# Performance work log

Hardware: AMD Instinct MI355X
Metric: run time of the kernel (lower is better)

Reference implementation:

```python
import jax, jax.numpy as jnp
import numpy as np

B, D, H, O, E = 16384, 256, 256, 256, 32
N_ACTIVE = 22          # int(32 * 0.7) from BoltzmannGate
TEMP = float(np.e)     # Boltzmann temperature
EPS = 1e-8


def setup_inputs() -> dict:
    key = jax.random.key(0)
    ks = jax.random.split(key, 7)
    s = 0.02  # init scale for weights
    return {
        "x":  jax.random.normal(ks[0], (B, D), dtype=jnp.float32),
        "W1": jax.random.normal(ks[1], (E, H, D), dtype=jnp.float32) * s,  # [E, out=H, in=D] torch Linear layout
        "b1": jax.random.normal(ks[2], (E, H), dtype=jnp.float32) * s,
        "W2": jax.random.normal(ks[3], (E, O, H), dtype=jnp.float32) * s,
        "b2": jax.random.normal(ks[4], (E, O), dtype=jnp.float32) * s,
        "Wg": jax.random.normal(ks[5], (E, D), dtype=jnp.float32) * s,
        "bg": jax.random.normal(ks[6], (E,), dtype=jnp.float32) * s,
    }


def reference(x, W1, b1, W2, b2, Wg, bg):
    # Dense all-experts forward: [B, E, H] -> relu -> [B, E, O]
    h = jax.nn.relu(jnp.einsum('bd,ehd->beh', x, W1) + b1[None, :, :])
    expert_out = jnp.einsum('beh,eoh->beo', h, W2) + b2[None, :, :]

    # Boltzmann gate: softmax(scores / T), keep top-k probs, renormalize.
    scores = (x @ Wg.T + bg) / TEMP                      # [B, E]
    probs = jax.nn.softmax(scores, axis=-1)
    _, topk_idx = jax.lax.top_k(probs, N_ACTIVE)         # [B, N_ACTIVE]
    mask = jnp.zeros_like(probs).at[jnp.arange(B)[:, None], topk_idx].set(1.0)
    weights = probs * mask
    weights = weights / (jnp.sum(weights, axis=-1, keepdims=True) + EPS)

    # Weighted combine over experts: [B, O]
    return jnp.einsum('be,beo->bo', weights, expert_out)
```

## Files before the change

kernel.cpp:

```cpp
#include <hip/hip_runtime.h>
#include <hip/hip_bf16.h>


typedef __attribute__((ext_vector_type(8))) short bf16x8;
typedef __attribute__((ext_vector_type(4))) float f32x4;

__device__ __forceinline__ unsigned short f2bf(float f) {
    unsigned u = __builtin_bit_cast(unsigned, f);
    u += 0x7FFFu + ((u >> 16) & 1u);
    return (unsigned short)(u >> 16);
}
__device__ __forceinline__ unsigned pack_bf16x2(float a, float b) {
    return (unsigned)f2bf(a) | ((unsigned)f2bf(b) << 16);
}

#define LX(r, ch) (((r) << 8) + ((((ch) ^ ((r) & 7))) << 3))

__global__ __launch_bounds__(256) void cvt_w(const float* __restrict__ W1,
                                             const float* __restrict__ W2,
                                             unsigned short* __restrict__ Wr) {
    int T = blockIdx.x * 256 + threadIdx.x;
    int lane = T & 63, t = (T >> 6) & 1, kb = (T >> 7) & 7;
    int s = (T >> 10) & 15, e = T >> 14;
    int l15 = lane & 15, quad = lane >> 4;
    int row = (s & 7) * 32 + t * 16 + l15;
    const float* src = ((s < 8) ? W1 : W2) +
                       ((long)e * 256 + row) * 256 + kb * 32 + quad * 8;
    float4 v0 = ((const float4*)src)[0], v1 = ((const float4*)src)[1];
    uint4 o;
    o.x = pack_bf16x2(v0.x, v0.y); o.y = pack_bf16x2(v0.z, v0.w);
    o.z = pack_bf16x2(v1.x, v1.y); o.w = pack_bf16x2(v1.z, v1.w);
    ((uint4*)Wr)[T] = o;
}

__global__ __launch_bounds__(1024, 4) void moe_kernel(
    const float* __restrict__ x,
    const unsigned short* __restrict__ Wr,
    const float* __restrict__ bias1,
    const float* __restrict__ b2,
    const float* __restrict__ Wg,
    const float* __restrict__ bg,
    float* __restrict__ out)
{
    __shared__ __align__(16) unsigned short x_s[64 * 256];
    __shared__ __align__(16) unsigned short h_s[2][64 * 256];
    __shared__ float gws[64 * 33];

    const int tid  = threadIdx.x;
    const int wv   = tid >> 6, lane = tid & 63;
    const int quad = lane >> 4, l15 = lane & 15;
    const int crew = wv >> 3, g = wv & 7;
    const int row0 = blockIdx.x * 64;

#pragma unroll
    for (int c = 0; c < 2; ++c) {
        int chunk = tid + c * 1024;
        int r = chunk >> 5, ch = chunk & 31;
        const float4* s = (const float4*)(x + (long)(row0 + r) * 256 + ch * 8);
        float4 v0 = s[0], v1 = s[1];
        uint4 o;
        o.x = pack_bf16x2(v0.x, v0.y); o.y = pack_bf16x2(v0.z, v0.w);
        o.z = pack_bf16x2(v1.x, v1.y); o.w = pack_bf16x2(v1.z, v1.w);
        *(uint4*)(&x_s[LX(r, ch)]) = o;
    }

    {
        const int e32 = lane & 31, half = lane >> 5;
        const float4* wg4 = (const float4*)(Wg + e32 * 256 + half * 128);
        float bgv = bg[e32];
        for (int i = 0; i < 4; ++i) {
            int lr = wv * 4 + i;
            const float4* xr4 = (const float4*)(x + (long)(row0 + lr) * 256 + half * 128);
            float acc = 0.f;
#pragma unroll
            for (int tt = 0; tt < 32; ++tt) {
                float4 w = wg4[tt], xv = xr4[tt];
                acc = fmaf(w.x, xv.x, acc); acc = fmaf(w.y, xv.y, acc);
                acc = fmaf(w.z, xv.z, acc); acc = fmaf(w.w, xv.w, acc);
            }
            acc += __shfl_xor(acc, 32);
            float score = (acc + bgv) / 2.71828182845904523f;

            float m = score;
#pragma unroll
            for (int d = 16; d >= 1; d >>= 1) m = fmaxf(m, __shfl_xor(m, d));
            float p = expf(score - m);
            float ps = p;
#pragma unroll
            for (int d = 16; d >= 1; d >>= 1) ps += __shfl_xor(ps, d);
            float prob = p / ps;

            int rank = 0;
#pragma unroll
            for (int j = 0; j < 32; ++j) {
                float pj = __shfl(prob, j);
                rank += (pj > prob || (pj == prob && j < e32)) ? 1 : 0;
            }
            float kept = (rank < 22) ? prob : 0.f;
            float wsum = kept;
#pragma unroll
            for (int d = 16; d >= 1; d >>= 1) wsum += __shfl_xor(wsum, d);
            float weight = kept / (wsum + 1e-8f);

            if (half == 0) gws[lr * 33 + e32] = weight;
        }
    }

    __syncthreads();

    f32x4 oacc[2][4];
#pragma unroll
    for (int ot = 0; ot < 2; ++ot)
#pragma unroll
        for (int rt = 0; rt < 4; ++rt) {
            f32x4 z = {0.f, 0.f, 0.f, 0.f};
            oacc[ot][rt] = z;
        }
    if (crew == 1) {
        for (int ee = 0; ee < 32; ++ee) {
            float gv[4];
#pragma unroll
            for (int rt = 0; rt < 4; ++rt) gv[rt] = gws[(rt * 16 + l15) * 33 + ee];
#pragma unroll
            for (int ot = 0; ot < 2; ++ot) {
                float4 bb = *(const float4*)(b2 + ee * 256 + g * 32 + ot * 16 + quad * 4);
#pragma unroll
                for (int rt = 0; rt < 4; ++rt) {
                    oacc[ot][rt][0] = fmaf(gv[rt], bb.x, oacc[ot][rt][0]);
                    oacc[ot][rt][1] = fmaf(gv[rt], bb.y, oacc[ot][rt][1]);
                    oacc[ot][rt][2] = fmaf(gv[rt], bb.z, oacc[ot][rt][2]);
                    oacc[ot][rt][3] = fmaf(gv[rt], bb.w, oacc[ot][rt][3]);
                }
            }
        }
    }

    bf16x8 buf[2][2];
    {
        const unsigned short* p0 = Wr + (long)wv * 8192;
        buf[0][0] = *(const bf16x8*)(p0 + lane * 8);
        buf[0][1] = *(const bf16x8*)(p0 + 512 + lane * 8);
        buf[1][0] = *(const bf16x8*)(p0 + 1024 + lane * 8);
        buf[1][1] = *(const bf16x8*)(p0 + 1536 + lane * 8);
    }

    for (int e = 0; e <= 32; ++e) {
        if (crew == 0) {
            if (e < 32) {
                f32x4 hacc[2][4];
#pragma unroll
                for (int ht = 0; ht < 2; ++ht)
#pragma unroll
                    for (int rt = 0; rt < 4; ++rt) {
                        f32x4 z = {0.f, 0.f, 0.f, 0.f};
                        hacc[ht][rt] = z;
                    }
                const unsigned short* w_e = Wr + ((long)(e * 16 + wv) * 8) * 1024;
#pragma unroll
                for (int kb = 0; kb < 8; ++kb) {
                    bf16x8 a0 = buf[kb & 1][0], a1 = buf[kb & 1][1];
                    const unsigned short* np =
                        w_e + ((kb < 6) ? (kb + 2) : (128 + kb - 6)) * 1024;
                    buf[kb & 1][0] = *(const bf16x8*)(np + lane * 8);
                    buf[kb & 1][1] = *(const bf16x8*)(np + 512 + lane * 8);
                    bf16x8 bbv[4];
#pragma unroll
                    for (int rt = 0; rt < 4; ++rt)
                        bbv[rt] = *(const bf16x8*)(&x_s[LX(rt * 16 + l15, kb * 4 + quad)]);
                    __builtin_amdgcn_s_setprio(1);
#pragma unroll
                    for (int rt = 0; rt < 4; ++rt) {
                        hacc[0][rt] = __builtin_amdgcn_mfma_f32_16x16x32_bf16(
                            a0, bbv[rt], hacc[0][rt], 0, 0, 0);
                        hacc[1][rt] = __builtin_amdgcn_mfma_f32_16x16x32_bf16(
                            a1, bbv[rt], hacc[1][rt], 0, 0, 0);
                    }
                    __builtin_amdgcn_s_setprio(0);
                }
                unsigned short* hb = h_s[e & 1];
                float4 bv[2]; float gw[4];
#pragma unroll
                for (int ht = 0; ht < 2; ++ht)
                    bv[ht] = *(const float4*)(bias1 + e * 256 + g * 32 + ht * 16 + quad * 4);
#pragma unroll
                for (int rt = 0; rt < 4; ++rt)
                    gw[rt] = gws[(rt * 16 + l15) * 33 + e];
#pragma unroll
                for (int ht = 0; ht < 2; ++ht) {
                    int hcol = g * 32 + ht * 16 + quad * 4;
                    int ch = hcol >> 3, off = hcol & 7;
#pragma unroll
                    for (int rt = 0; rt < 4; ++rt) {
                        int r = rt * 16 + l15;
                        float v0 = fmaxf(hacc[ht][rt][0] + bv[ht].x, 0.f) * gw[rt];
                        float v1 = fmaxf(hacc[ht][rt][1] + bv[ht].y, 0.f) * gw[rt];
                        float v2 = fmaxf(hacc[ht][rt][2] + bv[ht].z, 0.f) * gw[rt];
                        float v3 = fmaxf(hacc[ht][rt][3] + bv[ht].w, 0.f) * gw[rt];
                        uint2 pk;
                        pk.x = pack_bf16x2(v0, v1);
                        pk.y = pack_bf16x2(v2, v3);
                        *(uint2*)(&hb[(r << 8) + ((ch ^ (r & 7)) << 3) + off]) = pk;
                    }
                }
            }
        } else {
            if (e >= 1) {
                const int me = e - 1;
                const unsigned short* w_e = Wr + ((long)(me * 16 + wv) * 8) * 1024;
                const unsigned short* hbuf = h_s[me & 1];
#pragma unroll
                for (int kb = 0; kb < 8; ++kb) {
                    bf16x8 a0 = buf[kb & 1][0], a1 = buf[kb & 1][1];
                    const unsigned short* np =
                        w_e + ((kb < 6) ? (kb + 2) : (128 + kb - 6)) * 1024;
                    buf[kb & 1][0] = *(const bf16x8*)(np + lane * 8);
                    buf[kb & 1][1] = *(const bf16x8*)(np + 512 + lane * 8);
                    bf16x8 bbv[4];
#pragma unroll
                    for (int rt = 0; rt < 4; ++rt)
                        bbv[rt] = *(const bf16x8*)(&hbuf[LX(rt * 16 + l15, kb * 4 + quad)]);
                    __builtin_amdgcn_s_setprio(1);
#pragma unroll
                    for (int rt = 0; rt < 4; ++rt) {
                        oacc[0][rt] = __builtin_amdgcn_mfma_f32_16x16x32_bf16(
                            a0, bbv[rt], oacc[0][rt], 0, 0, 0);
                        oacc[1][rt] = __builtin_amdgcn_mfma_f32_16x16x32_bf16(
                            a1, bbv[rt], oacc[1][rt], 0, 0, 0);
                    }
                    __builtin_amdgcn_s_setprio(0);
                }
            }
        }

        __syncthreads();
    }

    if (crew == 1) {
#pragma unroll
        for (int ot = 0; ot < 2; ++ot)
#pragma unroll
            for (int rt = 0; rt < 4; ++rt)
                *(f32x4*)(out + (long)(row0 + rt * 16 + l15) * 256 +
                          g * 32 + ot * 16 + quad * 4) = oacc[ot][rt];
    }
}

extern "C" void kernel_launch(void* const* d_in, const int* in_sizes, int n_in,
                              void* d_out, int out_size, void* d_ws, size_t ws_size,
                              hipStream_t stream) {
    (void)in_sizes; (void)n_in; (void)out_size; (void)ws_size;
    const float* x  = (const float*)d_in[0];
    const float* W1 = (const float*)d_in[1];
    const float* b1 = (const float*)d_in[2];
    const float* W2 = (const float*)d_in[3];
    const float* b2 = (const float*)d_in[4];
    const float* Wg = (const float*)d_in[5];
    const float* bg = (const float*)d_in[6];
    float* out = (float*)d_out;

    unsigned short* Wr = (unsigned short*)d_ws;

    cvt_w<<<2048, 256, 0, stream>>>(W1, W2, Wr);
    moe_kernel<<<256, 1024, 0, stream>>>(x, Wr, b1, b2, Wg, bg, out);
}
```

Measured before the change: 304.8 us.

## Merge GEMM1/GEMM2 crews so every wave interleaves both stages per expert

Before, the 16 waves were split into two crews: one computed the first GEMM (hidden) and the other the second GEMM (output). Now every wave handles a 16-column slice of both, interleaving GEMM1 for expert e with GEMM2 for expert e-1 inside one k-loop. The aim is to balance MFMA load across all waves and hide each stage's latency with the other's instructions. The converted weight layout becomes a per-wave contiguous stream padded to 33 experts, with a 4-deep register prefetch ring. The full __syncthreads is swapped for an explicit lgkmcnt wait plus s_barrier, and the b2 bias prologue is now spread over all waves.

Measured after the change: 546.6 us. 79.3% more time.

```diff
diff --git a/kernel.cpp b/kernel.cpp
--- a/kernel.cpp
+++ b/kernel.cpp
@@ -20,18 +20,48 @@
                                              const float* __restrict__ W2,
                                              unsigned short* __restrict__ Wr) {
     int T = blockIdx.x * 256 + threadIdx.x;
-    int lane = T & 63, t = (T >> 6) & 1, kb = (T >> 7) & 7;
-    int s = (T >> 10) & 15, e = T >> 14;
+    int lane = T & 63, kb = (T >> 6) & 7, e = (T >> 9) & 31;
+    int s = (T >> 14) & 15, m = T >> 18;
     int l15 = lane & 15, quad = lane >> 4;
-    int row = (s & 7) * 32 + t * 16 + l15;
-    const float* src = ((s < 8) ? W1 : W2) +
-                       ((long)e * 256 + row) * 256 + kb * 32 + quad * 8;
+    const float* src = (m ? W2 : W1) +
+                       ((long)e * 256 + s * 16 + l15) * 256 + kb * 32 + quad * 8;
     float4 v0 = ((const float4*)src)[0], v1 = ((const float4*)src)[1];
     uint4 o;
     o.x = pack_bf16x2(v0.x, v0.y); o.y = pack_bf16x2(v0.z, v0.w);
     o.z = pack_bf16x2(v1.x, v1.y); o.w = pack_bf16x2(v1.z, v1.w);
-    ((uint4*)Wr)[T] = o;
-}
+    long U = (((long)(m * 16 + s) * 33 + e) * 8 + kb) * 64 + lane;
+    ((uint4*)Wr)[U] = o;
+}
+
+#define G1STEP(kb) do {                                                        \
+    bf16x8 a = r1[(kb) & 3];                                                   \
+    r1[(kb) & 3] = *(const bf16x8*)(w1p + (e * 8 + (kb) + 4) * 512);           \
+    bf16x8 xb0 = *(const bf16x8*)(&x_s[LX(l15,      (kb) * 4 + quad)]);        \
+    bf16x8 xb1 = *(const bf16x8*)(&x_s[LX(16 + l15, (kb) * 4 + quad)]);        \
+    bf16x8 xb2 = *(const bf16x8*)(&x_s[LX(32 + l15, (kb) * 4 + quad)]);        \
+    bf16x8 xb3 = *(const bf16x8*)(&x_s[LX(48 + l15, (kb) * 4 + quad)]);        \
+    __builtin_amdgcn_s_setprio(1);                                             \
+    hacc[0] = __builtin_amdgcn_mfma_f32_16x16x32_bf16(a, xb0, hacc[0], 0, 0, 0); \
+    hacc[1] = __builtin_amdgcn_mfma_f32_16x16x32_bf16(a, xb1, hacc[1], 0, 0, 0); \
+    hacc[2] = __builtin_amdgcn_mfma_f32_16x16x32_bf16(a, xb2, hacc[2], 0, 0, 0); \
+    hacc[3] = __builtin_amdgcn_mfma_f32_16x16x32_bf16(a, xb3, hacc[3], 0, 0, 0); \
+    __builtin_amdgcn_s_setprio(0);                                             \
+} while (0)
+
+#define G2STEP(kb) do {                                                        \
+    bf16x8 a = r2[(kb) & 3];                                                   \
+    r2[(kb) & 3] = *(const bf16x8*)(w2p + (me * 8 + (kb) + 4) * 512);          \
+    bf16x8 hb0 = *(const bf16x8*)(&hbr[LX(l15,      (kb) * 4 + quad)]);        \
+    bf16x8 hb1 = *(const bf16x8*)(&hbr[LX(16 + l15, (kb) * 4 + quad)]);        \
+    bf16x8 hb2 = *(const bf16x8*)(&hbr[LX(32 + l15, (kb) * 4 + quad)]);        \
+    bf16x8 hb3 = *(const bf16x8*)(&hbr[LX(48 + l15, (kb) * 4 + quad)]);        \
+    __builtin_amdgcn_s_setprio(1);                                             \
+    oacc[0] = __builtin_amdgcn_mfma_f32_16x16x32_bf16(a, hb0, oacc[0], 0, 0, 0); \
+    oacc[1] = __builtin_amdgcn_mfma_f32_16x16x32_bf16(a, hb1, oacc[1], 0, 0, 0); \
+    oacc[2] = __builtin_amdgcn_mfma_f32_16x16x32_bf16(a, hb2, oacc[2], 0, 0, 0); \
+    oacc[3] = __builtin_amdgcn_mfma_f32_16x16x32_bf16(a, hb3, oacc[3], 0, 0, 0); \
+    __builtin_amdgcn_s_setprio(0);                                             \
+} while (0)
 
 __global__ __launch_bounds__(1024, 4) void moe_kernel(
     const float* __restrict__ x,
@@ -49,7 +79,6 @@
     const int tid  = threadIdx.x;
     const int wv   = tid >> 6, lane = tid & 63;
     const int quad = lane >> 4, l15 = lane & 15;
-    const int crew = wv >> 3, g = wv & 7;
     const int row0 = blockIdx.x * 64;
 
 #pragma unroll
@@ -108,141 +137,81 @@
 
     __syncthreads();
 
-    f32x4 oacc[2][4];
-#pragma unroll
-    for (int ot = 0; ot < 2; ++ot)
+    const unsigned short* w1p = Wr + (long)wv * 33 * 4096 + lane * 8;
+    const unsigned short* w2p = Wr + (long)(16 + wv) * 33 * 4096 + lane * 8;
+    bf16x8 r1[4], r2[4];
+#pragma unroll
+    for (int t = 0; t < 4; ++t) {
+        r1[t] = *(const bf16x8*)(w1p + t * 512);
+        r2[t] = *(const bf16x8*)(w2p + t * 512);
+    }
+
+    f32x4 oacc[4];
+#pragma unroll
+    for (int rt = 0; rt < 4; ++rt) {
+        f32x4 z = {0.f, 0.f, 0.f, 0.f};
+        oacc[rt] = z;
+    }
+    for (int ee = 0; ee < 32; ++ee) {
+        float4 bb = *(const float4*)(b2 + ee * 256 + wv * 16 + quad * 4);
+#pragma unroll
+        for (int rt = 0; rt < 4; ++rt) {
+            float gv = gws[(rt * 16 + l15) * 33 + ee];
+            oacc[rt][0] = fmaf(gv, bb.x, oacc[rt][0]);
+            oacc[rt][1] = fmaf(gv, bb.y, oacc[rt][1]);
+            oacc[rt][2] = fmaf(gv, bb.z, oacc[rt][2]);
+            oacc[rt][3] = fmaf(gv, bb.w, oacc[rt][3]);
+        }
+    }
+
+    for (int e = 0; e <= 32; ++e) {
+        f32x4 hacc[4];
 #pragma unroll
         for (int rt = 0; rt < 4; ++rt) {
             f32x4 z = {0.f, 0.f, 0.f, 0.f};
-            oacc[ot][rt] = z;
-        }
-    if (crew == 1) {
-        for (int ee = 0; ee < 32; ++ee) {
-            float gv[4];
-#pragma unroll
-            for (int rt = 0; rt < 4; ++rt) gv[rt] = gws[(rt * 16 + l15) * 33 + ee];
-#pragma unroll
-            for (int ot = 0; ot < 2; ++ot) {
-                float4 bb = *(const float4*)(b2 + ee * 256 + g * 32 + ot * 16 + quad * 4);
-#pragma unroll
-                for (int rt = 0; rt < 4; ++rt) {
-                    oacc[ot][rt][0] = fmaf(gv[rt], bb.x, oacc[ot][rt][0]);
-                    oacc[ot][rt][1] = fmaf(gv[rt], bb.y, oacc[ot][rt][1]);
-                    oacc[ot][rt][2] = fmaf(gv[rt], bb.z, oacc[ot][rt][2]);
-                    oacc[ot][rt][3] = fmaf(gv[rt], bb.w, oacc[ot][rt][3]);
-                }
+            hacc[rt] = z;
+        }
+        const int me = e - 1;
+        const unsigned short* hbr = h_s[(e + 1) & 1];
+
+        if (e == 0) {
+#pragma unroll
+            for (int kb = 0; kb < 8; ++kb) G1STEP(kb);
+        } else if (e < 32) {
+#pragma unroll
+            for (int kb = 0; kb < 8; ++kb) { G1STEP(kb); G2STEP(kb); }
+        } else {
+#pragma unroll
+            for (int kb = 0; kb < 8; ++kb) G2STEP(kb);
+        }
+
+        if (e < 32) {
+            float4 bv = *(const float4*)(bias1 + e * 256 + wv * 16 + quad * 4);
+            unsigned short* hw = h_s[e & 1];
+            int ch = wv * 2 + (quad >> 1), off = (quad & 1) * 4;
+#pragma unroll
+            for (int rt = 0; rt < 4; ++rt) {
+                int r = rt * 16 + l15;
+                float gw = gws[r * 33 + e];
+                float v0 = fmaxf(hacc[rt][0] + bv.x, 0.f) * gw;
+                float v1 = fmaxf(hacc[rt][1] + bv.y, 0.f) * gw;
+                float v2 = fmaxf(hacc[rt][2] + bv.z, 0.f) * gw;
+                float v3 = fmaxf(hacc[rt][3] + bv.w, 0.f) * gw;
+                uint2 pk;
+                pk.x = pack_bf16x2(v0, v1);
+                pk.y = pack_bf16x2(v2, v3);
+                *(uint2*)(&hw[(r << 8) + ((ch ^ (r & 7)) << 3) + off]) = pk;
             }
         }
-    }
-
-    bf16x8 buf[2][2];
-    {
-        const unsigned short* p0 = Wr + (long)wv * 8192;
-        buf[0][0] = *(const bf16x8*)(p0 + lane * 8);
-        buf[0][1] = *(const bf16x8*)(p0 + 512 + lane * 8);
-        buf[1][0] = *(const bf16x8*)(p0 + 1024 + lane * 8);
-        buf[1][1] = *(const bf16x8*)(p0 + 1536 + lane * 8);
-    }
-
-    for (int e = 0; e <= 32; ++e) {
-        if (crew == 0) {
-            if (e < 32) {
-                f32x4 hacc[2][4];
-#pragma unroll
-                for (int ht = 0; ht < 2; ++ht)
-#pragma unroll
-                    for (int rt = 0; rt < 4; ++rt) {
-                        f32x4 z = {0.f, 0.f, 0.f, 0.f};
-                        hacc[ht][rt] = z;
-                    }
-                const unsigned short* w_e = Wr + ((long)(e * 16 + wv) * 8) * 1024;
-#pragma unroll
-                for (int kb = 0; kb < 8; ++kb) {
-                    bf16x8 a0 = buf[kb & 1][0], a1 = buf[kb & 1][1];
-                    const unsigned short* np =
-                        w_e + ((kb < 6) ? (kb + 2) : (128 + kb - 6)) * 1024;
-                    buf[kb & 1][0] = *(const bf16x8*)(np + lane * 8);
-                    buf[kb & 1][1] = *(const bf16x8*)(np + 512 + lane * 8);
-                    bf16x8 bbv[4];
-#pragma unroll
-                    for (int rt = 0; rt < 4; ++rt)
-                        bbv[rt] = *(const bf16x8*)(&x_s[LX(rt * 16 + l15, kb * 4 + quad)]);
-                    __builtin_amdgcn_s_setprio(1);
-#pragma unroll
-                    for (int rt = 0; rt < 4; ++rt) {
-                        hacc[0][rt] = __builtin_amdgcn_mfma_f32_16x16x32_bf16(
-                            a0, bbv[rt], hacc[0][rt], 0, 0, 0);
-                        hacc[1][rt] = __builtin_amdgcn_mfma_f32_16x16x32_bf16(
-                            a1, bbv[rt], hacc[1][rt], 0, 0, 0);
-                    }
-                    __builtin_amdgcn_s_setprio(0);
-                }
-                unsigned short* hb = h_s[e & 1];
-                float4 bv[2]; float gw[4];
-#pragma unroll
-                for (int ht = 0; ht < 2; ++ht)
-                    bv[ht] = *(const float4*)(bias1 + e * 256 + g * 32 + ht * 16 + quad * 4);
-#pragma unroll
-                for (int rt = 0; rt < 4; ++rt)
-                    gw[rt] = gws[(rt * 16 + l15) * 33 + e];
-#pragma unroll
-                for (int ht = 0; ht < 2; ++ht) {
-                    int hcol = g * 32 + ht * 16 + quad * 4;
-                    int ch = hcol >> 3, off = hcol & 7;
-#pragma unroll
-                    for (int rt = 0; rt < 4; ++rt) {
-                        int r = rt * 16 + l15;
-                        float v0 = fmaxf(hacc[ht][rt][0] + bv[ht].x, 0.f) * gw[rt];
-                        float v1 = fmaxf(hacc[ht][rt][1] + bv[ht].y, 0.f) * gw[rt];
-                        float v2 = fmaxf(hacc[ht][rt][2] + bv[ht].z, 0.f) * gw[rt];
-                        float v3 = fmaxf(hacc[ht][rt][3] + bv[ht].w, 0.f) * gw[rt];
-                        uint2 pk;
-                        pk.x = pack_bf16x2(v0, v1);
-                        pk.y = pack_bf16x2(v2, v3);
-                        *(uint2*)(&hb[(r << 8) + ((ch ^ (r & 7)) << 3) + off]) = pk;
-                    }
-                }
-            }
-        } else {
-            if (e >= 1) {
-                const int me = e - 1;
-                const unsigned short* w_e = Wr + ((long)(me * 16 + wv) * 8) * 1024;
-                const unsigned short* hbuf = h_s[me & 1];
-#pragma unroll
-                for (int kb = 0; kb < 8; ++kb) {
-                    bf16x8 a0 = buf[kb & 1][0], a1 = buf[kb & 1][1];
-                    const unsigned short* np =
-                        w_e + ((kb < 6) ? (kb + 2) : (128 + kb - 6)) * 1024;
-                    buf[kb & 1][0] = *(const bf16x8*)(np + lane * 8);
-                    buf[kb & 1][1] = *(const bf16x8*)(np + 512 + lane * 8);
-                    bf16x8 bbv[4];
-#pragma unroll
-                    for (int rt = 0; rt < 4; ++rt)
-                        bbv[rt] = *(const bf16x8*)(&hbuf[LX(rt * 16 + l15, kb * 4 + quad)]);
-                    __builtin_amdgcn_s_setprio(1);
-#pragma unroll
-                    for (int rt = 0; rt < 4; ++rt) {
-                        oacc[0][rt] = __builtin_amdgcn_mfma_f32_16x16x32_bf16(
-                            a0, bbv[rt], oacc[0][rt], 0, 0, 0);
-                        oacc[1][rt] = __builtin_amdgcn_mfma_f32_16x16x32_bf16(
-                            a1, bbv[rt], oacc[1][rt], 0, 0, 0);
-                    }
-                    __builtin_amdgcn_s_setprio(0);
-                }
-            }
-        }
-
-        __syncthreads();
-    }
-
-    if (crew == 1) {
-#pragma unroll
-        for (int ot = 0; ot < 2; ++ot)
-#pragma unroll
-            for (int rt = 0; rt < 4; ++rt)
-                *(f32x4*)(out + (long)(row0 + rt * 16 + l15) * 256 +
-                          g * 32 + ot * 16 + quad * 4) = oacc[ot][rt];
-    }
+
+        asm volatile("s_waitcnt lgkmcnt(0)" ::: "memory");
+        __builtin_amdgcn_s_barrier();
+    }
+
+#pragma unroll
+    for (int rt = 0; rt < 4; ++rt)
+        *(f32x4*)(out + (long)(row0 + rt * 16 + l15) * 256 +
+                  wv * 16 + quad * 4) = oacc[rt];
 }
 
 extern "C" void kernel_launch(void* const* d_in, const int* in_sizes, int n_in,
```
